# Optimization experiments

Hardware: AMD Instinct MI355X
Metric: run time of the kernel (lower is better)

## Reference

```python
import jax, jax.numpy as jnp
import numpy as np

N = 588   # node count, fixed by GRUCell(588, 64) input size
E = 9408  # edges = N * avg_degree 16
NEG = 0.01  # leaky_relu default slope
THRESH = 1.0 - 0.001


def setup_inputs() -> dict:
    key = jax.random.key(0)
    ks = jax.random.split(key, 20)
    w = lambda k, shape: (jax.random.normal(k, shape, dtype=jnp.float32) * 0.05)
    return {
        "features": jax.random.normal(ks[0], (N, 4), dtype=jnp.float32),
        "src": jax.random.randint(ks[1], (E,), 0, N),
        "dst": jax.random.randint(ks[2], (E,), 0, N),
        # CustomConv linears (sum-aggregate then Linear)
        "W1": w(ks[3], (4, 64)),  "b1": jnp.zeros((64,), jnp.float32),
        "W2": w(ks[4], (64, 64)), "b2": jnp.zeros((64,), jnp.float32),
        "W3": w(ks[5], (64, 1)),  "b3": jnp.zeros((1,), jnp.float32),
        "W5": w(ks[6], (64, 3)),  "b5": jnp.zeros((3,), jnp.float32),
        # GRUCell(588, 64): torch layout weight_ih [3*64, 588], weight_hh [3*64, 64]
        "gru_wi": w(ks[7], (192, 588)),
        "gru_wh": w(ks[8], (192, 64)),
        "gru_bi": jnp.zeros((192,), jnp.float32),
        "gru_bh": jnp.zeros((192,), jnp.float32),
        # end_determine Linear(64, 1)
        "w_end": w(ks[9], (64, 1)),
        "b_end": jnp.zeros((1,), jnp.float32),
        "cap": 30,
    }


def _lrelu(v):
    return jnp.where(v >= 0, v, NEG * v)


def reference(features, src, dst, W1, b1, W2, b2, W3, b3, W5, b5,
              gru_wi, gru_wh, gru_bi, gru_bh, w_end, b_end, cap):
    def conv(h, W, b):  # CustomConv: sum neighbors -> Linear
        agg = jax.ops.segment_sum(h[src], dst, num_segments=N)
        return agg @ W + b

    def gru(x, h):  # torch GRUCell, gate order r, z, n
        gx = x @ gru_wi.T + gru_bi          # [1, 192]
        gh = h @ gru_wh.T + gru_bh          # [1, 192]
        xr, xz, xn = jnp.split(gx, 3, axis=-1)
        hr, hz, hn = jnp.split(gh, 3, axis=-1)
        r = jax.nn.sigmoid(xr + hr)
        z = jax.nn.sigmoid(xz + hz)
        n = jnp.tanh(xn + r * hn)
        return (1.0 - z) * n + z * h

    state0 = jnp.zeros((1, 64), jnp.float32)
    x = _lrelu(conv(features, W1, b1))                 # [N, 64]
    inputt = _lrelu(conv(x, W3, b3)).T                 # [1, N]
    # NOTE: self.state is updated once before the loop, never inside it.
    state = gru(inputt, state0)                        # [1, 64]
    preprob = state @ w_end + b_end                    # [1, 1]
    fprob0 = jax.nn.sigmoid(preprob)
    s0 = jnp.sum(fprob0)                               # sum of sigmoid(probm)

    def step(carry, _):
        xc, s, fprob, counter = carry
        active = s < THRESH
        xn = _lrelu(conv(xc, W2, b2))                  # [N, 64]
        stn = gru(_lrelu(conv(xn, W3, b3)).T, state)   # uses frozen self.state
        pre = stn @ w_end + b_end                      # [1, 1]
        pr = jax.nn.sigmoid(pre)
        xc = jnp.where(active, xn, xc)
        fprob = jnp.where(active, pr, fprob)
        s = s + jnp.where(active, jnp.sum(pr), 0.0)
        counter = counter + active.astype(jnp.int32)
        return (xc, s, fprob, counter), None

    (x_last, _, fprob, counter), _ = jax.lax.scan(
        step, (x, s0, fprob0, jnp.int32(0)), None, length=int(cap))

    out = conv(x_last, W5, b5)                         # layer5, no activation: [N, 3]
    return out, counter, fprob
```

## Files before the change

kernel.cpp:

```cpp
#include <hip/hip_runtime.h>
#include <math.h>

#define NN 588
#define EE 9408
#define HD 64
#define NBLK 32
#define NTHR 1024
#define NWAVE (NTHR/64)
#define GXROWS (192/NBLK)
#define NEGS 0.01f
#define THRESHV 0.999f
#define MAGIC 0x51CAFE17u
#define DROW NN
#define EPADCAP 13536

struct Ctrl {
  unsigned ready;  unsigned pad0[15];
  unsigned xflags[NBLK*16];
  unsigned gflags[NBLK*16];
};

__device__ __forceinline__ float lrelu(float v){ return v >= 0.f ? v : NEGS*v; }
__device__ __forceinline__ float sigm(float v){ return 1.f/(1.f+expf(-v)); }
__device__ __forceinline__ float rdlane(float v, int l){
  return __int_as_float(__builtin_amdgcn_readlane(__float_as_int(v), l));
}
__device__ __forceinline__ float wredsum(float v){
  v += __shfl_down(v,32); v += __shfl_down(v,16); v += __shfl_down(v,8);
  v += __shfl_down(v,4);  v += __shfl_down(v,2);  v += __shfl_down(v,1);
  return v;
}
__device__ __forceinline__ void stga(float* p, float v){
  __hip_atomic_store(p, v, __ATOMIC_RELAXED, __HIP_MEMORY_SCOPE_AGENT);
}
__device__ __forceinline__ float ldga(const float* p){
  return __hip_atomic_load(p, __ATOMIC_RELAXED, __HIP_MEMORY_SCOPE_AGENT);
}
__device__ __forceinline__ void sink4(float4 v){
  asm volatile("" :: "v"(v.x), "v"(v.y), "v"(v.z), "v"(v.w));
}
__device__ __forceinline__ void prefetch_region(const float* p0, int nfloats, int t, int T){
  const float4* p = (const float4*)p0;
  const int n = nfloats >> 2;
  for (int base = t; base < n; base += T*8) {
    float4 v[8];
    #pragma unroll
    for (int u = 0; u < 8; ++u) { int i = base + u*T; if (i >= n) i = n - 1; v[u] = p[i]; }
    #pragma unroll
    for (int u = 0; u < 8; ++u) sink4(v[u]);
  }
}

__device__ __forceinline__ void barrive(unsigned* flags, int bid, unsigned gen) {
  __syncthreads();
  if (threadIdx.x == 0) {
    __hip_atomic_store(&flags[bid*16], gen, __ATOMIC_RELEASE, __HIP_MEMORY_SCOPE_AGENT);
  }
}
__device__ __forceinline__ void bwait(unsigned* flags, unsigned gen) {
  if ((threadIdx.x >> 6) == 0) {
    int lane = threadIdx.x & 63;
    const unsigned* fp = &flags[lane*16];
    long bail = 0;
    for (;;) {
      int ok = (lane >= NBLK) ? 1 :
               (__hip_atomic_load(fp, __ATOMIC_RELAXED, __HIP_MEMORY_SCOPE_AGENT) >= gen);
      if (__all(ok)) break;
      __builtin_amdgcn_s_sleep(1);
      if (++bail > (1L<<22)) break;
    }
    asm volatile("" ::: "memory");
  }
  __syncthreads();
}

__global__ __launch_bounds__(NTHR)
void lastgcn_kernel(const float* __restrict__ feat, const int* __restrict__ src,
                    const int* __restrict__ dst,
                    const float* __restrict__ W1, const float* __restrict__ b1,
                    const float* __restrict__ W2, const float* __restrict__ b2,
                    const float* __restrict__ W3, const float* __restrict__ b3,
                    const float* __restrict__ W5, const float* __restrict__ b5,
                    const float* __restrict__ wi, const float* __restrict__ wh,
                    const float* __restrict__ bi, const float* __restrict__ bh,
                    const float* __restrict__ w_end, const float* __restrict__ b_end,
                    const int* __restrict__ capp,
                    float* __restrict__ out, Ctrl* ctrl,
                    float* __restrict__ x0g, float* __restrict__ x1g,
                    float* __restrict__ ypub, float* __restrict__ gxpub) {
  const int tid  = threadIdx.x;
  const int lane = tid & 63;
  const int w    = tid >> 6;
  const int bid  = blockIdx.x;
  const int nbeg = (NN*bid)/NBLK;
  const int nend = (NN*(bid+1))/NBLK;
  const int cnt  = nend - nbeg;
  const int r0   = bid*GXROWS;

  __shared__ float  W2L[64*64];
  __shared__ unsigned short eidxL[EPADCAP];
  __shared__ int    offL[NN+1];
  __shared__ int    curL[NN];
  __shared__ float  yF[NN+1];
  __shared__ float  inpF[NN];
  __shared__ float  ghL[192];
  __shared__ float4 f4L[80];
  __shared__ int    wsumL[NWAVE];

  if (bid == 0) {
    if (tid < HD) { stga(&x0g[DROW*HD + tid], 0.f); stga(&x1g[DROW*HD + tid], 0.f); }
    if (tid == 64) stga(&ypub[NN], 0.f);
    if (tid == 65) stga(&ypub[(NN+1) + NN], 0.f);
    for (int i2 = tid; i2 < NBLK*32; i2 += NTHR) {
      ((unsigned*)ctrl)[16 + i2] = 0u;
    }
    __syncthreads();
    if (tid == 0) {
      __threadfence();
      __hip_atomic_store(&ctrl->ready, MAGIC, __ATOMIC_RELEASE, __HIP_MEMORY_SCOPE_AGENT);
    }
  } else if (tid == 0) {
    long bail = 0;
    while (__hip_atomic_load(&ctrl->ready, __ATOMIC_RELAXED, __HIP_MEMORY_SCOPE_AGENT) != MAGIC) {
      __builtin_amdgcn_s_sleep(1);
      if (++bail > (1L<<24)) break;
    }
    __threadfence();
  }
  __syncthreads();

  for (int i = tid; i < NN; i += NTHR) curL[i] = 0;
  for (int i = tid; i < 1024; i += NTHR) ((float4*)W2L)[i] = ((const float4*)W2)[i];
  __syncthreads();
  if (w < 8) {
    for (int e = tid; e < EE; e += 512) atomicAdd(&curL[dst[e]], 1);
  } else {
    const int pt = tid - 512, PT = 512;
    prefetch_region(wi + r0*NN, GXROWS*NN, pt, PT);
    prefetch_region(wh, 192*64, pt, PT);
    prefetch_region(w_end, 64, pt, PT);
  }
  __syncthreads();

  {
    const int n0 = 2*tid, n1 = n0 + 1;
    int d0 = (n0 < NN) ? curL[n0] : 0;
    int d1 = (n1 < NN) ? curL[n1] : 0;
    int p0 = (d0 + 7) & ~7, p1 = (d1 + 7) & ~7;
    int my = p0 + p1;
    int inc = my;
    for (int o = 1; o < 64; o <<= 1) { int u = __shfl_up(inc, o); if (lane >= o) inc += u; }
    if (lane == 63) wsumL[w] = inc;
    __syncthreads();
    if (w == 0 && lane < NWAVE) {
      int s0 = wsumL[lane];
      int is = s0;
      for (int o = 1; o < NWAVE; o <<= 1) { int u = __shfl_up(is, o); if (lane >= o) is += u; }
      wsumL[lane] = is - s0;
    }
    __syncthreads();
    int base = wsumL[w] + inc - my;
    if (n0 < NN) { offL[n0] = base;      curL[n0] = base;      }
    if (n1 < NN) { offL[n1] = base + p0; curL[n1] = base + p0; }
    if (tid == NTHR-1) offL[NN] = base + p0 + p1;
  }
  __syncthreads();
  for (int e = tid; e < EE; e += NTHR) {
    int p = atomicAdd(&curL[dst[e]], 1);
    eidxL[p] = (unsigned short)src[e];
  }
  __syncthreads();
  {
    const int n0 = 2*tid, n1 = n0 + 1;
    if (n0 < NN) for (int k = curL[n0]; k < offL[n0+1]; ++k) eidxL[k] = (unsigned short)DROW;
    if (n1 < NN) for (int k = curL[n1]; k < offL[n1+1]; ++k) eidxL[k] = (unsigned short)DROW;
  }
  __syncthreads();

  if (tid < cnt) {
    int n = nbeg + tid;
    int o = offL[n], o1 = offL[n+1];
    float fx=0.f, fy=0.f, fz=0.f, fw2=0.f;
    for (int k = o; k < o1; k += 8) {
      uint4 q = *(const uint4*)(eidxL + k);
      int id[8] = { (int)(q.x & 0xFFFF), (int)(q.x >> 16), (int)(q.y & 0xFFFF), (int)(q.y >> 16),
                    (int)(q.z & 0xFFFF), (int)(q.z >> 16), (int)(q.w & 0xFFFF), (int)(q.w >> 16) };
      float4 tv[8]; float m[8];
      #pragma unroll
      for (int u = 0; u < 8; ++u) {
        int valid = id[u] < NN;
        m[u] = valid ? 1.f : 0.f;
        tv[u] = *(const float4*)(feat + (valid ? id[u] : 0)*4);
      }
      #pragma unroll
      for (int u = 0; u < 8; ++u) { fx += m[u]*tv[u].x; fy += m[u]*tv[u].y; fz += m[u]*tv[u].z; fw2 += m[u]*tv[u].w; }
    }
    f4L[tid] = make_float4(fx, fy, fz, fw2);
  }
  __syncthreads();
  const float W3r = W3[lane];
  for (int i = w; i < cnt; i += NWAVE) {
    int n = nbeg + i; float4 f = f4L[i];
    float v = b1[lane] + f.x*W1[lane] + f.y*W1[64+lane] + f.z*W1[128+lane] + f.w*W1[192+lane];
    v = lrelu(v);
    stga(&x0g[n*HD + lane], v);
    float yv = wredsum(v * W3r);
    if (lane == 0) stga(&ypub[n], yv);
  }
  barrive(ctrl->xflags, bid, 1u);

  const float b3v  = b3[0];
  const float b2r  = b2[lane];
  const float bend0 = b_end[0];
  const float wer  = w_end[lane];
  const int cap = capp[0];
  float* xc = x0g;
  float* xn = x1g;

  float stj = 0.f;
  float s_run = 0.f;
  float fprobr = 0.f;
  int   nsteps = 0;

  for (int k = 0; ; ++k) {
    bwait(ctrl->xflags, (unsigned)(k+1));
    const float* yp = ypub + (k&1)*(NN+1);
    for (int i = tid; i <= NN; i += NTHR) yF[i] = ldga(&yp[i]);

    if (k >= 1) {
      const float* gxp = gxpub + ((k-1)&1)*192;
      int j = lane;
      float gxr = ldga(&gxp[j]), gxz = ldga(&gxp[64+j]), gxn2 = ldga(&gxp[128+j]);
      if (k == 1) {
        float r  = sigm(gxr + bh[j]);
        float z  = sigm(gxz + bh[64+j]);
        float n2 = tanhf(gxn2 + r*bh[128+j]);
        float st = (1.f - z)*n2;
        stj = st;
        float t2 = wredsum(st * wer);
        float pr = sigm(rdlane(t2,0) + bend0);
        s_run = pr; fprobr = pr; nsteps = 0;
        for (int rr = w; rr < 192; rr += NWAVE) {
          float p = wredsum(wh[rr*64 + lane] * stj);
          if (lane == 0) ghL[rr] = p + bh[rr];
        }
        __syncthreads();
      } else {
        float r  = sigm(gxr + ghL[j]);
        float z  = sigm(gxz + ghL[64+j]);
        float n2 = tanhf(gxn2 + r*ghL[128+j]);
        float st = (1.f - z)*n2 + z*stj;
        float t2 = wredsum(st * wer);
        float pr = sigm(rdlane(t2,0) + bend0);
        s_run += pr; fprobr = pr; nsteps = k-1;
      }
      if (s_run >= THRESHV || k == cap+1) break;
    }

    if (k < cap) {
      float* ypn = ypub + ((k+1)&1)*(NN+1);
      for (int i = w; i < cnt; i += 2*NWAVE) {
        int i2 = i + NWAVE;
        bool has2 = (i2 < cnt);
        int nA = nbeg + i, nB = nbeg + (has2 ? i2 : i);
        int oA = offL[nA], lA = offL[nA+1] - oA;
        int oB = offL[nB], lB = offL[nB+1] - oB;
        float accA = 0.f, accB = 0.f;
        int pcm = lA > lB ? lA : lB;
        for (int kk = 0; kk < pcm; kk += 8) {
          float ta[8], tb[8];
          if (kk < lA) {
            uint4 q = *(const uint4*)(eidxL + oA + kk);
            ta[0] = ldga(&xc[(int)(q.x & 0xFFFF)*HD + lane]); ta[1] = ldga(&xc[(int)(q.x >> 16)*HD + lane]);
            ta[2] = ldga(&xc[(int)(q.y & 0xFFFF)*HD + lane]); ta[3] = ldga(&xc[(int)(q.y >> 16)*HD + lane]);
            ta[4] = ldga(&xc[(int)(q.z & 0xFFFF)*HD + lane]); ta[5] = ldga(&xc[(int)(q.z >> 16)*HD + lane]);
            ta[6] = ldga(&xc[(int)(q.w & 0xFFFF)*HD + lane]); ta[7] = ldga(&xc[(int)(q.w >> 16)*HD + lane]);
          } else { for (int u = 0; u < 8; ++u) ta[u] = 0.f; }
          if (kk < lB) {
            uint4 q = *(const uint4*)(eidxL + oB + kk);
            tb[0] = ldga(&xc[(int)(q.x & 0xFFFF)*HD + lane]); tb[1] = ldga(&xc[(int)(q.x >> 16)*HD + lane]);
            tb[2] = ldga(&xc[(int)(q.y & 0xFFFF)*HD + lane]); tb[3] = ldga(&xc[(int)(q.y >> 16)*HD + lane]);
            tb[4] = ldga(&xc[(int)(q.z & 0xFFFF)*HD + lane]); tb[5] = ldga(&xc[(int)(q.z >> 16)*HD + lane]);
            tb[6] = ldga(&xc[(int)(q.w & 0xFFFF)*HD + lane]); tb[7] = ldga(&xc[(int)(q.w >> 16)*HD + lane]);
          } else { for (int u = 0; u < 8; ++u) tb[u] = 0.f; }
          #pragma unroll
          for (int u = 0; u < 8; ++u) { accA += ta[u]; accB += tb[u]; }
        }
        float a0=0.f,a1=0.f,a2=0.f,a3=0.f, c0=0.f,c1=0.f,c2=0.f,c3=0.f;
        #pragma unroll
        for (int l = 0; l < 64; l += 4) {
          float w0 = W2L[(l+0)*64 + lane];
          float w1v = W2L[(l+1)*64 + lane];
          float w2v = W2L[(l+2)*64 + lane];
          float w3v = W2L[(l+3)*64 + lane];
          a0 = fmaf(rdlane(accA,l+0), w0,  a0);  c0 = fmaf(rdlane(accB,l+0), w0,  c0);
          a1 = fmaf(rdlane(accA,l+1), w1v, a1);  c1 = fmaf(rdlane(accB,l+1), w1v, c1);
          a2 = fmaf(rdlane(accA,l+2), w2v, a2);  c2 = fmaf(rdlane(accB,l+2), w2v, c2);
          a3 = fmaf(rdlane(accA,l+3), w3v, a3);  c3 = fmaf(rdlane(accB,l+3), w3v, c3);
        }
        {
          float vA = lrelu(b2r + (a0+a1)+(a2+a3));
          stga(&xn[nA*HD + lane], vA);
          float yv = wredsum(vA * W3r);
          if (lane == 0) stga(&ypn[nA], yv);
        }
        if (has2) {
          float vB = lrelu(b2r + (c0+c1)+(c2+c3));
          stga(&xn[nB*HD + lane], vB);
          float yv = wredsum(vB * W3r);
          if (lane == 0) stga(&ypn[nB], yv);
        }
      }
    }
    __syncthreads();

    for (int n = tid; n < NN; n += NTHR) {
      int o = offL[n], o1 = offL[n+1];
      float a = 0.f;
      for (int kk = o; kk < o1; kk += 8) {
        uint4 q = *(const uint4*)(eidxL + kk);
        a += yF[q.x & 0xFFFF] + yF[q.x >> 16] + yF[q.y & 0xFFFF] + yF[q.y >> 16];
        a += yF[q.z & 0xFFFF] + yF[q.z >> 16] + yF[q.w & 0xFFFF] + yF[q.w >> 16];
      }
      inpF[n] = lrelu(a + b3v);
    }
    __syncthreads();

    {
      float* gxp = gxpub + (k&1)*192;
      const float4* inp4 = (const float4*)inpF;
      for (int rr = w; rr < GXROWS; rr += NWAVE) {
        const float4* row4 = (const float4*)(wi + (r0 + rr)*NN);
        float p = 0.f;
        #pragma unroll
        for (int kk = 0; kk < 3; ++kk) {
          int c = lane + (kk << 6);
          if (c < 147) {
            float4 a = row4[c], b = inp4[c];
            p += a.x*b.x + a.y*b.y + a.z*b.z + a.w*b.w;
          }
        }
        p = wredsum(p);
        if (lane == 0) stga(&gxp[r0 + rr], p + bi[r0 + rr]);
      }
    }

    barrive(ctrl->xflags, bid, (unsigned)(k+2));
    { float* t = xc; xc = xn; xn = t; }
  }

  float* xf = xn;
  for (int i = w; i < cnt; i += NWAVE) {
    int n = nbeg + i;
    int o = offL[n], o1 = offL[n+1];
    float acc = 0.f;
    for (int k = o; k < o1; k += 8) {
      uint4 q = *(const uint4*)(eidxL + k);
      float t[8];
      t[0] = ldga(&xf[(int)(q.x & 0xFFFF)*HD + lane]); t[1] = ldga(&xf[(int)(q.x >> 16)*HD + lane]);
      t[2] = ldga(&xf[(int)(q.y & 0xFFFF)*HD + lane]); t[3] = ldga(&xf[(int)(q.y >> 16)*HD + lane]);
      t[4] = ldga(&xf[(int)(q.z & 0xFFFF)*HD + lane]); t[5] = ldga(&xf[(int)(q.z >> 16)*HD + lane]);
      t[6] = ldga(&xf[(int)(q.w & 0xFFFF)*HD + lane]); t[7] = ldga(&xf[(int)(q.w >> 16)*HD + lane]);
      #pragma unroll
      for (int u = 0; u < 8; ++u) acc += t[u];
    }
    float p0 = wredsum(acc * W5[lane*3 + 0]);
    float p1 = wredsum(acc * W5[lane*3 + 1]);
    float p2 = wredsum(acc * W5[lane*3 + 2]);
    if (lane == 0) {
      out[n*3 + 0] = p0 + b5[0];
      out[n*3 + 1] = p1 + b5[1];
      out[n*3 + 2] = p2 + b5[2];
    }
  }
  if (bid == 0 && tid == 0) {
    out[NN*3]     = (float)nsteps;
    out[NN*3 + 1] = fprobr;
  }
}

extern "C" void kernel_launch(void* const* d_in, const int* in_sizes, int n_in,
                              void* d_out, int out_size, void* d_ws, size_t ws_size,
                              hipStream_t stream) {
  const float* feat  = (const float*)d_in[0];
  const int*   src   = (const int*)d_in[1];
  const int*   dst   = (const int*)d_in[2];
  const float* W1    = (const float*)d_in[3];
  const float* b1    = (const float*)d_in[4];
  const float* W2    = (const float*)d_in[5];
  const float* b2    = (const float*)d_in[6];
  const float* W3    = (const float*)d_in[7];
  const float* b3    = (const float*)d_in[8];
  const float* W5    = (const float*)d_in[9];
  const float* b5    = (const float*)d_in[10];
  const float* wi    = (const float*)d_in[11];
  const float* wh    = (const float*)d_in[12];
  const float* bi    = (const float*)d_in[13];
  const float* bh    = (const float*)d_in[14];
  const float* w_end = (const float*)d_in[15];
  const float* b_end = (const float*)d_in[16];
  const int*   capp  = (const int*)d_in[17];

  float* out = (float*)d_out;
  char* wsb = (char*)d_ws;
  Ctrl*  ctrl   = (Ctrl*)wsb;
  float* x0g    = (float*)(wsb + 8192);
  float* x1g    = x0g + (size_t)(NN+1)*HD;
  float* ypub   = x1g + (size_t)(NN+1)*HD;
  float* gxpub  = ypub + 2*(NN+1);

  lastgcn_kernel<<<dim3(NBLK), dim3(NTHR), 0, stream>>>(
      feat, src, dst, W1, b1, W2, b2, W3, b3, W5, b5,
      wi, wh, bi, bh, w_end, b_end, capp, out,
      ctrl, x0g, x1g, ypub, gxpub);
}
```

Measured before the change: 134.9 us.

## Stage packed edges in LDS, vectorize edge loads, defer gh matvec past barrier

The edge list is now read from global memory once with int4 loads and packed (src<<16|dst) into an LDS array while the degree histogram is built. The CSR scatter pass then reads from LDS instead of reloading src and dst from global. The prefetch of the wh matrix is dropped, and the one-time wh*state matvec that fills ghL moves from the critical path before the barrier to after it, so it can overlap with waiting on other blocks. Spin-wait bail-out limits are also reduced. The extra LDS array adds about 37KB, which could reduce occupancy or exceed the LDS limit, and the shorter bail-outs raise the risk of leaving a wait early.

```diff
diff --git a/kernel.cpp b/kernel.cpp
--- a/kernel.cpp
+++ b/kernel.cpp
@@ -67,7 +67,7 @@
                (__hip_atomic_load(fp, __ATOMIC_RELAXED, __HIP_MEMORY_SCOPE_AGENT) >= gen);
       if (__all(ok)) break;
       __builtin_amdgcn_s_sleep(1);
-      if (++bail > (1L<<22)) break;
+      if (++bail > (1L<<19)) break;
     }
     asm volatile("" ::: "memory");
   }
@@ -99,6 +99,7 @@
 
   __shared__ float  W2L[64*64];
   __shared__ unsigned short eidxL[EPADCAP];
+  __shared__ unsigned edgeL[EE];
   __shared__ int    offL[NN+1];
   __shared__ int    curL[NN];
   __shared__ float  yF[NN+1];
@@ -123,7 +124,7 @@
     long bail = 0;
     while (__hip_atomic_load(&ctrl->ready, __ATOMIC_RELAXED, __HIP_MEMORY_SCOPE_AGENT) != MAGIC) {
       __builtin_amdgcn_s_sleep(1);
-      if (++bail > (1L<<24)) break;
+      if (++bail > (1L<<22)) break;
     }
     __threadfence();
   }
@@ -132,13 +133,18 @@
   for (int i = tid; i < NN; i += NTHR) curL[i] = 0;
   for (int i = tid; i < 1024; i += NTHR) ((float4*)W2L)[i] = ((const float4*)W2)[i];
   __syncthreads();
-  if (w < 8) {
-    for (int e = tid; e < EE; e += 512) atomicAdd(&curL[dst[e]], 1);
-  } else {
-    const int pt = tid - 512, PT = 512;
-    prefetch_region(wi + r0*NN, GXROWS*NN, pt, PT);
-    prefetch_region(wh, 192*64, pt, PT);
-    prefetch_region(w_end, 64, pt, PT);
+  {
+    const int4* s4 = (const int4*)src;
+    const int4* d4 = (const int4*)dst;
+    for (int e4 = tid; e4 < EE/4; e4 += NTHR) {
+      int4 s = s4[e4], d = d4[e4];
+      edgeL[e4*4+0] = (unsigned)((s.x<<16)|d.x); atomicAdd(&curL[d.x],1);
+      edgeL[e4*4+1] = (unsigned)((s.y<<16)|d.y); atomicAdd(&curL[d.y],1);
+      edgeL[e4*4+2] = (unsigned)((s.z<<16)|d.z); atomicAdd(&curL[d.z],1);
+      edgeL[e4*4+3] = (unsigned)((s.w<<16)|d.w); atomicAdd(&curL[d.w],1);
+    }
+    prefetch_region(wi + r0*NN, GXROWS*NN, tid, NTHR);
+    prefetch_region(w_end, 64, tid, NTHR);
   }
   __syncthreads();
 
@@ -165,9 +171,13 @@
     if (tid == NTHR-1) offL[NN] = base + p0 + p1;
   }
   __syncthreads();
-  for (int e = tid; e < EE; e += NTHR) {
-    int p = atomicAdd(&curL[dst[e]], 1);
-    eidxL[p] = (unsigned short)src[e];
+  for (int e4 = tid; e4 < EE/4; e4 += NTHR) {
+    uint4 pk = ((const uint4*)edgeL)[e4];
+    int p;
+    p = atomicAdd(&curL[pk.x & 0xFFFF], 1); eidxL[p] = (unsigned short)(pk.x >> 16);
+    p = atomicAdd(&curL[pk.y & 0xFFFF], 1); eidxL[p] = (unsigned short)(pk.y >> 16);
+    p = atomicAdd(&curL[pk.z & 0xFFFF], 1); eidxL[p] = (unsigned short)(pk.z >> 16);
+    p = atomicAdd(&curL[pk.w & 0xFFFF], 1); eidxL[p] = (unsigned short)(pk.w >> 16);
   }
   __syncthreads();
   {
@@ -240,11 +250,6 @@
         float t2 = wredsum(st * wer);
         float pr = sigm(rdlane(t2,0) + bend0);
         s_run = pr; fprobr = pr; nsteps = 0;
-        for (int rr = w; rr < 192; rr += NWAVE) {
-          float p = wredsum(wh[rr*64 + lane] * stj);
-          if (lane == 0) ghL[rr] = p + bh[rr];
-        }
-        __syncthreads();
       } else {
         float r  = sigm(gxr + ghL[j]);
         float z  = sigm(gxz + ghL[64+j]);
@@ -346,6 +351,13 @@
     }
 
     barrive(ctrl->xflags, bid, (unsigned)(k+2));
+
+    if (k == 1) {
+      for (int rr = w; rr < 192; rr += NWAVE) {
+        float p = wredsum(wh[rr*64 + lane] * stj);
+        if (lane == 0) ghL[rr] = p + bh[rr];
+      }
+    }
     { float* t = xc; xc = xn; xn = t; }
   }
 
```

Measured after the change: 134.2 us. Within noise of the previous version (-0.5%).
